# Optimization experiments

Measured on AMD Instinct MI355X. Metric: run time of the kernel, lower is better.

## Reference

```python
import jax, jax.numpy as jnp
import numpy as np

SCALING = 2.0      # lora_alpha / r = 32 / 16
TEMPERATURE = 1.0  # router_temperature


def setup_inputs() -> dict:
    key = jax.random.key(0)
    ks = jax.random.split(key, 7)
    B, S, D, K, R = 4, 2048, 4096, 8, 16
    # Note: torch inits lora_B to zeros; we use small random values so the
    return {
        "x": jax.random.normal(ks[0], (B, S, D), dtype=jnp.float32),
        "base_w": jax.random.normal(ks[1], (D, D), dtype=jnp.float32) * 0.02,
        "base_b": jax.random.normal(ks[2], (D,), dtype=jnp.float32) * 0.02,
        "lora_A": jax.random.normal(ks[3], (K, R, D), dtype=jnp.float32) * 0.02,
        "lora_B": jax.random.normal(ks[4], (K, D, R), dtype=jnp.float32) * 0.02,
        "router_w": jax.random.normal(ks[5], (K, D), dtype=jnp.float32) * 0.02,
        "router_b": jnp.zeros((K,), dtype=jnp.float32),
    }


def reference(x, base_w, base_b, lora_A, lora_B, router_w, router_b):
    # base_layer(x): x @ W^T + b
    base = jnp.einsum("bsd,od->bso", x, base_w) + base_b
    # router on mean-pooled sequence (x.dim()==3 branch): softmax(Linear(mean_s x))
    router_in = x.mean(axis=1)                                   # [B, D]
    logits = router_in @ router_w.T + router_b                   # [B, K]
    weights = jax.nn.softmax(logits / TEMPERATURE, axis=-1)      # [B, K]
    # grouped LoRA experts: h = A_k x, out = sum_k w_k * B_k h  (dropout p=0 -> identity)
    h = jnp.einsum("bsd,krd->bskr", x, lora_A)                   # [B, S, K, R]
    lora = jnp.einsum("bskr,kor,bk->bso", h, lora_B, weights)    # [B, S, D]
    return base + SCALING * lora
```

## Files before the change

kernel.cpp:

```cpp
#include <hip/hip_runtime.h>
#include <hip/hip_fp16.h>
#include <stdint.h>

typedef _Float16 f16;
typedef __attribute__((ext_vector_type(8))) _Float16 f16x8;
typedef __attribute__((ext_vector_type(4))) float f32x4;

#define D_DIM 4096
#define S_DIM 2048
#define M_DIM 8192
#define R_DIM 16
#define KR 128
#define KTOT 4224
#define NKT 66
#define SCALING 2.0f

#define WS_AP    0
#define WS_WP    69206016
#define WS_AH    103809024
#define WS_HP    104857600
#define WS_PART  121634816
#define WS_LG    123731968
#define WS_WS    123732096

__device__ __forceinline__ void load_lds16(const void* g, void* l) {
  __builtin_amdgcn_global_load_lds(
      (const __attribute__((address_space(1))) void*)g,
      (__attribute__((address_space(3))) void*)l, 16, 0, 0);
}

union H4 { f16 h[4]; ushort4 u; };

__global__ void conv_x(const float* __restrict__ x, f16* __restrict__ Ap,
                       float* __restrict__ part) {
  int rc = blockIdx.x;
  int cc = blockIdx.y;
  int col = cc * 1024 + threadIdx.x * 4;
  long base = (long)rc * 64 * D_DIM + col;
  float s0 = 0, s1 = 0, s2 = 0, s3 = 0;
  for (int r = 0; r < 64; ++r) {
    float4 v = *(const float4*)(x + base + (long)r * D_DIM);
    H4 t; t.h[0] = (f16)v.x; t.h[1] = (f16)v.y; t.h[2] = (f16)v.z; t.h[3] = (f16)v.w;
    *(ushort4*)((char*)Ap + ((long)(rc * 64 + r) * KTOT + col) * 2) = t.u;
    s0 += v.x; s1 += v.y; s2 += v.z; s3 += v.w;
  }
  float4 sv; sv.x = s0; sv.y = s1; sv.z = s2; sv.w = s3;
  *(float4*)(part + (long)rc * D_DIM + col) = sv;
}

__global__ void conv_w(const float* __restrict__ w, f16* __restrict__ Wp) {
  int rc = blockIdx.x;
  int cc = blockIdx.y;
  int col = cc * 1024 + threadIdx.x * 4;
  long base = (long)rc * 64 * D_DIM + col;
  for (int r = 0; r < 64; ++r) {
    float4 v = *(const float4*)(w + base + (long)r * D_DIM);
    H4 t; t.h[0] = (f16)v.x; t.h[1] = (f16)v.y; t.h[2] = (f16)v.z; t.h[3] = (f16)v.w;
    *(ushort4*)((char*)Wp + ((long)(rc * 64 + r) * KTOT + col) * 2) = t.u;
  }
}

__global__ void conv_bext(const float* __restrict__ loraB, f16* __restrict__ Wp) {
  int g = blockIdx.x * 256 + threadIdx.x;
  int n = g >> 7, kr = g & 127;
  int k = kr >> 4, r = kr & 15;
  float v = loraB[((long)k * D_DIM + n) * R_DIM + r];
  Wp[(long)n * KTOT + D_DIM + kr] = (f16)v;
}

__global__ void conv_aext(const float* __restrict__ loraA, f16* __restrict__ Ah) {
  long g = ((long)blockIdx.x * 256 + threadIdx.x) * 4;
  float4 v = *(const float4*)(loraA + g);
  H4 t; t.h[0] = (f16)v.x; t.h[1] = (f16)v.y; t.h[2] = (f16)v.z; t.h[3] = (f16)v.w;
  *(ushort4*)((char*)Ah + g * 2) = t.u;
}

__global__ void router_logits(const float* __restrict__ part, const float* __restrict__ rw,
                              const float* __restrict__ rb, float* __restrict__ logits) {
  int b = blockIdx.x >> 3, k = blockIdx.x & 7;
  const float* w = rw + k * D_DIM;
  float p = 0.f;
  for (int d = threadIdx.x; d < D_DIM; d += 256) {
    float s = 0.f;
    #pragma unroll 8
    for (int i = 0; i < 32; ++i) s += part[(long)(b * 32 + i) * D_DIM + d];
    p += s * w[d];
  }
  __shared__ float red[4];
  for (int off = 32; off; off >>= 1) p += __shfl_down(p, off);
  if ((threadIdx.x & 63) == 0) red[threadIdx.x >> 6] = p;
  __syncthreads();
  if (threadIdx.x == 0)
    logits[b * 8 + k] = (red[0] + red[1] + red[2] + red[3]) / (float)S_DIM + rb[k];
}

__global__ void router_softmax(const float* __restrict__ logits, float* __restrict__ wsc) {
  int lane = threadIdx.x;
  if (lane < 32) {
    float L = logits[lane];
    float m = L;
    m = fmaxf(m, __shfl_xor(m, 1));
    m = fmaxf(m, __shfl_xor(m, 2));
    m = fmaxf(m, __shfl_xor(m, 4));
    float e = __expf(L - m);
    float s = e;
    s += __shfl_xor(s, 1); s += __shfl_xor(s, 2); s += __shfl_xor(s, 4);
    wsc[lane] = e / s * SCALING;
  }
}

__global__ void combine_h(const float* __restrict__ hp, const float* __restrict__ wsc,
                          f16* __restrict__ Ap) {
  long g = (long)blockIdx.x * 256 + threadIdx.x;
  long row = g >> 7; int kr = (int)(g & 127);
  int b = (int)(row >> 11);
  float s = hp[g] + hp[g + 1048576] + hp[g + 2097152] + hp[g + 3145728];
  Ap[row * KTOT + D_DIM + kr] = (f16)(s * wsc[b * 8 + (kr >> 4)]);
}

__device__ __forceinline__ void stage256(const f16* __restrict__ G, long row0, int ld,
                                         long kbase, char* ldsT, int tid) {
  int lr = tid >> 3;
  int sw = (((tid & 7) * 16) ^ ((lr & 7) << 4)) >> 1;
  char* wbase = ldsT + ((tid >> 6) << 10);
  #pragma unroll
  for (int j = 0; j < 4; ++j) {
    const f16* g = G + (row0 + j * 64 + lr) * (long)ld + kbase + sw;
    load_lds16(g, wbase + j * 8192);
  }
}
__device__ __forceinline__ void stage128(const f16* __restrict__ G, long row0, int ld,
                                         long kbase, char* ldsT, int tid) {
  int lr = tid >> 3;
  int sw = (((tid & 7) * 16) ^ ((lr & 7) << 4)) >> 1;
  char* wbase = ldsT + ((tid >> 6) << 10);
  #pragma unroll
  for (int j = 0; j < 4; ++j) {
    const f16* g = G + (row0 + j * 32 + lr) * (long)ld + kbase + sw;
    load_lds16(g, wbase + j * 4096);
  }
}

__global__ __launch_bounds__(256, 2) void gemm_h2(
    const f16* __restrict__ A, int lda, const f16* __restrict__ Bt, int ldb,
    float* __restrict__ hp) {
  __shared__ __align__(16) char smem[65536];
  int tid = threadIdx.x;
  int wave = tid >> 6, lane = tid & 63;
  int wr = wave >> 1, wc = wave & 1;
  int fr = lane & 15, fq = lane >> 4;
  long row0 = (long)blockIdx.x * 128;
  long koff = (long)blockIdx.y * 1024;

  f32x4 acc[4][4] = {};

  stage128(A,  row0, lda, koff,      smem,         tid);
  stage128(Bt, 0,    ldb, koff,      smem + 16384, tid);
  stage128(A,  row0, lda, koff + 64, smem + 32768, tid);
  stage128(Bt, 0,    ldb, koff + 64, smem + 49152, tid);
  asm volatile("s_waitcnt vmcnt(8)" ::: "memory");
  asm volatile("s_barrier" ::: "memory");

  int cur = 0;
  int sw = (fr & 7) << 4;
  for (int t = 0; t < 16; ++t) {
    const char* Ab = smem + cur * 32768;
    const char* Bb = Ab + 16384;
    __builtin_amdgcn_s_setprio(1);
    #pragma unroll
    for (int ks = 0; ks < 2; ++ks) {
      int kb = ks * 64 + fq * 16;
      f16x8 af[4], bf[4];
      #pragma unroll
      for (int mi = 0; mi < 4; ++mi)
        af[mi] = *(const f16x8*)(Ab + (wr * 64 + mi * 16 + fr) * 128 + (kb ^ sw));
      #pragma unroll
      for (int ni = 0; ni < 4; ++ni)
        bf[ni] = *(const f16x8*)(Bb + (wc * 64 + ni * 16 + fr) * 128 + (kb ^ sw));
      #pragma unroll
      for (int mi = 0; mi < 4; ++mi)
        #pragma unroll
        for (int ni = 0; ni < 4; ++ni)
          acc[mi][ni] = __builtin_amdgcn_mfma_f32_16x16x32_f16(af[mi], bf[ni], acc[mi][ni], 0, 0, 0);
    }
    __builtin_amdgcn_s_setprio(0);
    asm volatile("s_barrier" ::: "memory");
    if (t + 2 < 16) {
      stage128(A,  row0, lda, koff + (t + 2) * 64, smem + cur * 32768,         tid);
      stage128(Bt, 0,    ldb, koff + (t + 2) * 64, smem + cur * 32768 + 16384, tid);
      asm volatile("s_waitcnt vmcnt(8)" ::: "memory");
    } else {
      asm volatile("s_waitcnt vmcnt(0)" ::: "memory");
    }
    asm volatile("s_barrier" ::: "memory");
    cur ^= 1;
  }

  long zb = (long)blockIdx.y * (long)M_DIM * 128;
  #pragma unroll
  for (int ni = 0; ni < 4; ++ni) {
    int col = wc * 64 + ni * 16 + fr;
    #pragma unroll
    for (int mi = 0; mi < 4; ++mi) {
      long row = row0 + wr * 64 + mi * 16 + fq * 4;
      float* cp = hp + zb + row * 128 + col;
      #pragma unroll
      for (int j = 0; j < 4; ++j) cp[(long)j * 128] = acc[mi][ni][j];
    }
  }
}

__global__ __launch_bounds__(512, 2) void gemm256(
    const f16* __restrict__ A, int lda, const f16* __restrict__ Bt, int ldb,
    int nkt, const float* __restrict__ bias, float* __restrict__ C, int ldc) {
  __shared__ __align__(16) char smem[131072];
  int tid = threadIdx.x;
  int wave = tid >> 6, lane = tid & 63;
  int wr = wave >> 2, wc = wave & 3;
  int fr = lane & 15, fq = lane >> 4;

  int flat = blockIdx.x;
  int wg = (flat & 7) * 64 + (flat >> 3);
  long row0 = (long)(wg >> 4) * 256;
  long col0 = (long)(wg & 15) * 256;

  f32x4 acc[8][4] = {};

  stage256(A,  row0, lda, 0,  smem,          tid);
  stage256(Bt, col0, ldb, 0,  smem + 32768,  tid);
  stage256(A,  row0, lda, 64, smem + 65536,  tid);
  stage256(Bt, col0, ldb, 64, smem + 98304,  tid);
  asm volatile("s_waitcnt vmcnt(8)" ::: "memory");
  asm volatile("s_barrier" ::: "memory");

  int cur = 0;
  int sw = (fr & 7) << 4;
  for (int t = 0; t < nkt; ++t) {
    const char* Ab = smem + cur * 65536;
    const char* Bb = Ab + 32768;
    __builtin_amdgcn_s_setprio(1);
    #pragma unroll
    for (int qm = 0; qm < 2; ++qm) {
      f16x8 af[4][2];
      #pragma unroll
      for (int m2 = 0; m2 < 4; ++m2) {
        int row = wr * 128 + (qm * 4 + m2) * 16 + fr;
        af[m2][0] = *(const f16x8*)(Ab + row * 128 + ((fq * 16) ^ sw));
        af[m2][1] = *(const f16x8*)(Ab + row * 128 + ((64 + fq * 16) ^ sw));
      }
      #pragma unroll
      for (int qn = 0; qn < 2; ++qn) {
        f16x8 bf[2][2];
        #pragma unroll
        for (int n2 = 0; n2 < 2; ++n2) {
          int rowb = wc * 64 + (qn * 2 + n2) * 16 + fr;
          bf[n2][0] = *(const f16x8*)(Bb + rowb * 128 + ((fq * 16) ^ sw));
          bf[n2][1] = *(const f16x8*)(Bb + rowb * 128 + ((64 + fq * 16) ^ sw));
        }
        #pragma unroll
        for (int m2 = 0; m2 < 4; ++m2)
          #pragma unroll
          for (int n2 = 0; n2 < 2; ++n2) {
            f32x4* a = &acc[qm * 4 + m2][qn * 2 + n2];
            *a = __builtin_amdgcn_mfma_f32_16x16x32_f16(af[m2][0], bf[n2][0], *a, 0, 0, 0);
            *a = __builtin_amdgcn_mfma_f32_16x16x32_f16(af[m2][1], bf[n2][1], *a, 0, 0, 0);
          }
      }
    }
    __builtin_amdgcn_s_setprio(0);
    asm volatile("s_barrier" ::: "memory");
    if (t + 2 < nkt) {
      stage256(A,  row0, lda, (long)(t + 2) * 64, smem + cur * 65536,         tid);
      stage256(Bt, col0, ldb, (long)(t + 2) * 64, smem + cur * 65536 + 32768, tid);
      asm volatile("s_waitcnt vmcnt(8)" ::: "memory");
    } else {
      asm volatile("s_waitcnt vmcnt(0)" ::: "memory");
    }
    asm volatile("s_barrier" ::: "memory");
    cur ^= 1;
  }

  #pragma unroll
  for (int ni = 0; ni < 4; ++ni) {
    long col = col0 + wc * 64 + ni * 16 + fr;
    float bv = bias[col];
    #pragma unroll
    for (int mi = 0; mi < 8; ++mi) {
      long row = row0 + wr * 128 + mi * 16 + fq * 4;
      float* cp = C + row * ldc + col;
      #pragma unroll
      for (int j = 0; j < 4; ++j) cp[(long)j * ldc] = acc[mi][ni][j] + bv;
    }
  }
}

extern "C" void kernel_launch(void* const* d_in, const int* in_sizes, int n_in,
                              void* d_out, int out_size, void* d_ws, size_t ws_size,
                              hipStream_t stream) {
  (void)in_sizes; (void)n_in; (void)out_size; (void)ws_size;
  const float* x        = (const float*)d_in[0];
  const float* base_w   = (const float*)d_in[1];
  const float* base_b   = (const float*)d_in[2];
  const float* lora_A   = (const float*)d_in[3];
  const float* lora_B   = (const float*)d_in[4];
  const float* router_w = (const float*)d_in[5];
  const float* router_b = (const float*)d_in[6];
  float* out = (float*)d_out;

  char* ws = (char*)d_ws;
  f16* Ap       = (f16*)(ws + WS_AP);
  f16* Wp       = (f16*)(ws + WS_WP);
  f16* Ah       = (f16*)(ws + WS_AH);
  float* hp     = (float*)(ws + WS_HP);
  float* part   = (float*)(ws + WS_PART);
  float* logits = (float*)(ws + WS_LG);
  float* wsc    = (float*)(ws + WS_WS);

  conv_x<<<dim3(128, 4), 256, 0, stream>>>(x, Ap, part);
  conv_w<<<dim3(64, 4), 256, 0, stream>>>(base_w, Wp);
  conv_bext<<<2048, 256, 0, stream>>>(lora_B, Wp);
  conv_aext<<<512, 256, 0, stream>>>(lora_A, Ah);
  router_logits<<<32, 256, 0, stream>>>(part, router_w, router_b, logits);
  router_softmax<<<1, 64, 0, stream>>>(logits, wsc);
  gemm_h2<<<dim3(64, 4), 256, 0, stream>>>(Ap, KTOT, Ah, D_DIM, hp);
  combine_h<<<4096, 256, 0, stream>>>(hp, wsc, Ap);
  gemm256<<<512, 512, 0, stream>>>(Ap, KTOT, Wp, KTOT, NKT, base_b, out, D_DIM);
}
```

Measured before the change: 588.7 us.

## Merge LoRA conversion kernels, drop setprio, restructure gemm256 fragment loop

Result: no change. 582.2 us (-1.1%).

```diff
diff --git a/kernel.cpp b/kernel.cpp
--- a/kernel.cpp
+++ b/kernel.cpp
@@ -60,19 +60,20 @@
   }
 }
 
-__global__ void conv_bext(const float* __restrict__ loraB, f16* __restrict__ Wp) {
-  int g = blockIdx.x * 256 + threadIdx.x;
-  int n = g >> 7, kr = g & 127;
-  int k = kr >> 4, r = kr & 15;
-  float v = loraB[((long)k * D_DIM + n) * R_DIM + r];
-  Wp[(long)n * KTOT + D_DIM + kr] = (f16)v;
-}
-
-__global__ void conv_aext(const float* __restrict__ loraA, f16* __restrict__ Ah) {
-  long g = ((long)blockIdx.x * 256 + threadIdx.x) * 4;
-  float4 v = *(const float4*)(loraA + g);
-  H4 t; t.h[0] = (f16)v.x; t.h[1] = (f16)v.y; t.h[2] = (f16)v.z; t.h[3] = (f16)v.w;
-  *(ushort4*)((char*)Ah + g * 2) = t.u;
+__global__ void conv_small(const float* __restrict__ loraB, const float* __restrict__ loraA,
+                           f16* __restrict__ Wp, f16* __restrict__ Ah) {
+  if (blockIdx.x < 2048) {
+    int g = blockIdx.x * 256 + threadIdx.x;
+    int n = g >> 7, kr = g & 127;
+    int k = kr >> 4, r = kr & 15;
+    float v = loraB[((long)k * D_DIM + n) * R_DIM + r];
+    Wp[(long)n * KTOT + D_DIM + kr] = (f16)v;
+  } else {
+    long g = ((long)(blockIdx.x - 2048) * 256 + threadIdx.x) * 4;
+    float4 v = *(const float4*)(loraA + g);
+    H4 t; t.h[0] = (f16)v.x; t.h[1] = (f16)v.y; t.h[2] = (f16)v.z; t.h[3] = (f16)v.w;
+    *(ushort4*)((char*)Ah + g * 2) = t.u;
+  }
 }
 
 __global__ void router_logits(const float* __restrict__ part, const float* __restrict__ rw,
@@ -118,6 +119,17 @@
   Ap[row * KTOT + D_DIM + kr] = (f16)(s * wsc[b * 8 + (kr >> 4)]);
 }
 
+__device__ __forceinline__ void stage128(const f16* __restrict__ G, long row0, int ld,
+                                         long kbase, char* ldsT, int tid) {
+  int lr = tid >> 3;
+  int sw = (((tid & 7) * 16) ^ ((lr & 7) << 4)) >> 1;
+  char* wbase = ldsT + ((tid >> 6) << 10);
+  #pragma unroll
+  for (int j = 0; j < 4; ++j) {
+    const f16* g = G + (row0 + j * 32 + lr) * (long)ld + kbase + sw;
+    load_lds16(g, wbase + j * 4096);
+  }
+}
 __device__ __forceinline__ void stage256(const f16* __restrict__ G, long row0, int ld,
                                          long kbase, char* ldsT, int tid) {
   int lr = tid >> 3;
@@ -127,17 +139,6 @@
   for (int j = 0; j < 4; ++j) {
     const f16* g = G + (row0 + j * 64 + lr) * (long)ld + kbase + sw;
     load_lds16(g, wbase + j * 8192);
-  }
-}
-__device__ __forceinline__ void stage128(const f16* __restrict__ G, long row0, int ld,
-                                         long kbase, char* ldsT, int tid) {
-  int lr = tid >> 3;
-  int sw = (((tid & 7) * 16) ^ ((lr & 7) << 4)) >> 1;
-  char* wbase = ldsT + ((tid >> 6) << 10);
-  #pragma unroll
-  for (int j = 0; j < 4; ++j) {
-    const f16* g = G + (row0 + j * 32 + lr) * (long)ld + kbase + sw;
-    load_lds16(g, wbase + j * 4096);
   }
 }
 
@@ -166,7 +167,6 @@
   for (int t = 0; t < 16; ++t) {
     const char* Ab = smem + cur * 32768;
     const char* Bb = Ab + 16384;
-    __builtin_amdgcn_s_setprio(1);
     #pragma unroll
     for (int ks = 0; ks < 2; ++ks) {
       int kb = ks * 64 + fq * 16;
@@ -183,7 +183,6 @@
         for (int ni = 0; ni < 4; ++ni)
           acc[mi][ni] = __builtin_amdgcn_mfma_f32_16x16x32_f16(af[mi], bf[ni], acc[mi][ni], 0, 0, 0);
     }
-    __builtin_amdgcn_s_setprio(0);
     asm volatile("s_barrier" ::: "memory");
     if (t + 2 < 16) {
       stage128(A,  row0, lda, koff + (t + 2) * 64, smem + cur * 32768,         tid);
@@ -238,36 +237,22 @@
   for (int t = 0; t < nkt; ++t) {
     const char* Ab = smem + cur * 65536;
     const char* Bb = Ab + 32768;
-    __builtin_amdgcn_s_setprio(1);
     #pragma unroll
-    for (int qm = 0; qm < 2; ++qm) {
-      f16x8 af[4][2];
-      #pragma unroll
-      for (int m2 = 0; m2 < 4; ++m2) {
-        int row = wr * 128 + (qm * 4 + m2) * 16 + fr;
-        af[m2][0] = *(const f16x8*)(Ab + row * 128 + ((fq * 16) ^ sw));
-        af[m2][1] = *(const f16x8*)(Ab + row * 128 + ((64 + fq * 16) ^ sw));
-      }
-      #pragma unroll
-      for (int qn = 0; qn < 2; ++qn) {
-        f16x8 bf[2][2];
+    for (int ks = 0; ks < 2; ++ks) {
+      int kb = ks * 64 + fq * 16;
+      f16x8 af[8], bf[4];
+      #pragma unroll
+      for (int n2 = 0; n2 < 4; ++n2)
+        bf[n2] = *(const f16x8*)(Bb + (wc * 64 + n2 * 16 + fr) * 128 + (kb ^ sw));
+      #pragma unroll
+      for (int m2 = 0; m2 < 8; ++m2)
+        af[m2] = *(const f16x8*)(Ab + (wr * 128 + m2 * 16 + fr) * 128 + (kb ^ sw));
+      #pragma unroll
+      for (int m2 = 0; m2 < 8; ++m2)
         #pragma unroll
-        for (int n2 = 0; n2 < 2; ++n2) {
-          int rowb = wc * 64 + (qn * 2 + n2) * 16 + fr;
-          bf[n2][0] = *(const f16x8*)(Bb + rowb * 128 + ((fq * 16) ^ sw));
-          bf[n2][1] = *(const f16x8*)(Bb + rowb * 128 + ((64 + fq * 16) ^ sw));
-        }
-        #pragma unroll
-        for (int m2 = 0; m2 < 4; ++m2)
-          #pragma unroll
-          for (int n2 = 0; n2 < 2; ++n2) {
-            f32x4* a = &acc[qm * 4 + m2][qn * 2 + n2];
-            *a = __builtin_amdgcn_mfma_f32_16x16x32_f16(af[m2][0], bf[n2][0], *a, 0, 0, 0);
-            *a = __builtin_amdgcn_mfma_f32_16x16x32_f16(af[m2][1], bf[n2][1], *a, 0, 0, 0);
-          }
-      }
-    }
-    __builtin_amdgcn_s_setprio(0);
+        for (int n2 = 0; n2 < 4; ++n2)
+          acc[m2][n2] = __builtin_amdgcn_mfma_f32_16x16x32_f16(af[m2], bf[n2], acc[m2][n2], 0, 0, 0);
+    }
     asm volatile("s_barrier" ::: "memory");
     if (t + 2 < nkt) {
       stage256(A,  row0, lda, (long)(t + 2) * 64, smem + cur * 65536,         tid);
@@ -318,8 +303,7 @@
 
   conv_x<<<dim3(128, 4), 256, 0, stream>>>(x, Ap, part);
   conv_w<<<dim3(64, 4), 256, 0, stream>>>(base_w, Wp);
-  conv_bext<<<2048, 256, 0, stream>>>(lora_B, Wp);
-  conv_aext<<<512, 256, 0, stream>>>(lora_A, Ah);
+  conv_small<<<2560, 256, 0, stream>>>(lora_B, lora_A, Wp, Ah);
   router_logits<<<32, 256, 0, stream>>>(part, router_w, router_b, logits);
   router_softmax<<<1, 64, 0, stream>>>(logits, wsc);
   gemm_h2<<<dim3(64, 4), 256, 0, stream>>>(Ap, KTOT, Ah, D_DIM, hp);
```
